# Kernel optimization log

Measured on AMD Instinct MI355X. Metric: run time of the kernel, lower is better.

Reference implementation:

```python
import jax, jax.numpy as jnp
import numpy as np

SEQ = 8192
D_IN = 1024
D_OUT = 128


def setup_inputs() -> dict:
    key = jax.random.key(0)
    k0, k1, k2, k3 = jax.random.split(key, 4)
    # kaiming-normal-ish init for weights (std = sqrt(2/fan_in))
    std = np.sqrt(2.0 / D_IN).astype(np.float32)
    return {
        "x": jax.random.normal(k0, (SEQ, D_IN), dtype=jnp.float32),
        "wq": jax.random.normal(k1, (D_IN, D_OUT), dtype=jnp.float32) * std,
        "wk": jax.random.normal(k2, (D_IN, D_OUT), dtype=jnp.float32) * std,
        "wv": jax.random.normal(k3, (D_IN, D_OUT), dtype=jnp.float32) * std,
    }


def reference(x, wq, wk, wv):
    # q,k,v: [S, d_out]
    q = x @ wq
    k = x @ wk
    v = x @ wv
    scale = jnp.sqrt(jnp.asarray(D_OUT, dtype=q.dtype))
    scores = (q @ k.T) / scale          # [S, S]
    attn = jax.nn.softmax(scores, axis=-1)
    return attn @ v                      # [S, d_out]
```

## Files before the change

### kernel.cpp

```cpp
#include <hip/hip_runtime.h>
#include <cstdint>

#define SEQ    8192
#define DIN    1024
#define DOUT   128
#define NSPLIT 8
#define KVTILE 64
#define QTILE  128
#define QK_SCALE 0.1275174246f
#define RESCALE_THR 8.0f

typedef unsigned short u16;
typedef __bf16 bf16x8 __attribute__((ext_vector_type(8)));
typedef float  f32x4  __attribute__((ext_vector_type(4)));
typedef float  f32x16 __attribute__((ext_vector_type(16)));
typedef unsigned short u16x8 __attribute__((ext_vector_type(8)));
typedef unsigned short u16x4 __attribute__((ext_vector_type(4)));
typedef unsigned int u32x2 __attribute__((ext_vector_type(2)));
typedef unsigned int u32x4 __attribute__((ext_vector_type(4)));

__device__ __forceinline__ u16 bfc(float f) {
  return __builtin_bit_cast(u16, (__bf16)f);
}
__device__ __forceinline__ float bf2f(u16 u) {
  union { uint32_t u; float f; } c; c.u = ((uint32_t)u) << 16; return c.f;
}

__device__ __forceinline__ bf16x8 ldsu8(const u16* base, int byteoff) {
  return __builtin_bit_cast(bf16x8,
    *reinterpret_cast<const u16x8*>(reinterpret_cast<const char*>(base) + byteoff));
}
__device__ __forceinline__ bf16x8 glbu8(const u16* p) {
  return __builtin_bit_cast(bf16x8, *reinterpret_cast<const u16x8*>(p));
}

__device__ __forceinline__ void gload_lds16(const void* g, void* l) {
  __builtin_amdgcn_global_load_lds(
      (const __attribute__((address_space(1))) void*)g,
      (__attribute__((address_space(3))) void*)l, 16, 0, 0);
}

__global__ __launch_bounds__(256) void k_wtrans(const float* __restrict__ wq,
                                                const float* __restrict__ wk,
                                                const float* __restrict__ wv,
                                                u16* __restrict__ Wt) {
  const float* w = (blockIdx.y == 0) ? wq : (blockIdx.y == 1) ? wk : wv;
  int idx = blockIdx.x * 256 + threadIdx.x;
  int k = idx >> 7, n = idx & 127;
  Wt[(size_t)blockIdx.y * (DOUT * DIN) + (size_t)n * DIN + k] = bfc(w[idx]);
}

__global__ __launch_bounds__(256) void k_xcast(const float* __restrict__ x,
                                               u16* __restrict__ Xb) {
  size_t base = ((size_t)blockIdx.x * 256 + threadIdx.x) * 8;
  float4 lo = *reinterpret_cast<const float4*>(x + base);
  float4 hi = *reinterpret_cast<const float4*>(x + base + 4);
  u16x8 v = { bfc(lo.x), bfc(lo.y), bfc(lo.z), bfc(lo.w),
              bfc(hi.x), bfc(hi.y), bfc(hi.z), bfc(hi.w) };
  *reinterpret_cast<u16x8*>(Xb + base) = v;
}

__global__ __launch_bounds__(256, 2) void k_gemm(const u16* __restrict__ Xb,
                                                 const u16* __restrict__ Wt,
                                                 u16* __restrict__ Q,
                                                 u16* __restrict__ K,
                                                 u16* __restrict__ Vt) {
  __shared__ __attribute__((aligned(16))) u16 As[2][64 * 128];
  __shared__ __attribute__((aligned(16))) u16 Bs[2][96 * 128];
  const int tid  = threadIdx.x;
  const int lane = tid & 63, wave = tid >> 6;
  const int lm   = lane & 15, g = lane >> 4;
  const int wm   = wave >> 1, wn = wave & 1;
  const int m0   = blockIdx.x * 64;
  const int n0   = blockIdx.y * 96;
  const int swzr = (lm & 7) << 4;

  const int trow = tid >> 4;
  const int tswz = ((tid & 15) << 4) ^ ((trow & 7) << 4);
  const char* baseA = (const char*)Xb + (size_t)(m0 + trow) * 2048 + tswz;
  const char* baseB = (const char*)Wt + (size_t)(n0 + trow) * 2048 + tswz;

  auto stage = [&](int buf, int kc) {
    const int kb = kc * 256;
#pragma unroll
    for (int i = 0; i < 4; ++i)
      gload_lds16(baseA + kb + i * 32768, &As[buf][i * 2048 + wave * 512]);
#pragma unroll
    for (int j = 0; j < 6; ++j)
      gload_lds16(baseB + kb + j * 32768, &Bs[buf][j * 2048 + wave * 512]);
  };

  f32x4 acc[2][3];
#pragma unroll
  for (int s = 0; s < 2; ++s)
#pragma unroll
    for (int nb = 0; nb < 3; ++nb) acc[s][nb] = (f32x4){0.f, 0.f, 0.f, 0.f};

  auto compute = [&](int buf) {
    const u16* As_ = As[buf];
    const u16* Bs_ = Bs[buf];
    bf16x8 a[2][4], b[3][4];
#pragma unroll
    for (int s = 0; s < 2; ++s)
#pragma unroll
      for (int t = 0; t < 4; ++t)
        a[s][t] = ldsu8(As_, (wm * 32 + s * 16 + lm) * 256 +
                             ((t * 64 + 16 * g) ^ swzr));
#pragma unroll
    for (int nb = 0; nb < 3; ++nb)
#pragma unroll
      for (int t = 0; t < 4; ++t)
        b[nb][t] = ldsu8(Bs_, (wn * 48 + nb * 16 + lm) * 256 +
                              ((t * 64 + 16 * g) ^ swzr));
#pragma unroll
    for (int s = 0; s < 2; ++s)
#pragma unroll
      for (int nb = 0; nb < 3; ++nb)
#pragma unroll
        for (int t = 0; t < 4; ++t)
          acc[s][nb] = __builtin_amdgcn_mfma_f32_16x16x32_bf16(
              a[s][t], b[nb][t], acc[s][nb], 0, 0, 0);
  };

  stage(0, 0);
  asm volatile("s_waitcnt vmcnt(0)" ::: "memory");
  __syncthreads();

#pragma unroll
  for (int kc = 0; kc < 8; kc += 2) {
    if (kc + 1 < 8) stage(1, kc + 1);
    compute(0);
    asm volatile("s_waitcnt vmcnt(0)" ::: "memory");
    __syncthreads();
    if (kc + 2 < 8) stage(0, kc + 2);
    compute(1);
    asm volatile("s_waitcnt vmcnt(0)" ::: "memory");
    __syncthreads();
  }

#pragma unroll
  for (int s = 0; s < 2; ++s)
#pragma unroll
    for (int nb = 0; nb < 3; ++nb) {
      int n = n0 + wn * 48 + nb * 16 + lm;
      int which = n >> 7, col = n & 127;
#pragma unroll
      for (int r = 0; r < 4; ++r) {
        int m = m0 + wm * 32 + s * 16 + g * 4 + r;
        if (which == 0)       Q[(size_t)m * DOUT + col] = bfc(acc[s][nb][r] * QK_SCALE);
        else if (which == 1)  K[(size_t)m * DOUT + col] = bfc(acc[s][nb][r]);
        else                  Vt[(size_t)col * SEQ + m] = bfc(acc[s][nb][r]);
      }
    }
}

__global__ __launch_bounds__(256, 2) void k_attn(const u16* __restrict__ Q,
                                                 const u16* __restrict__ K,
                                                 const u16* __restrict__ Vt,
                                                 u16* __restrict__ Op,
                                                 float* __restrict__ Mb,
                                                 float* __restrict__ Lb) {
  __shared__ __attribute__((aligned(16))) u16 Ks[2][64 * 128];
  __shared__ __attribute__((aligned(16))) u16 Vts[2][128 * 64];
  const int tid  = threadIdx.x;
  const int lane = tid & 63, wave = tid >> 6;
  const int l31  = lane & 31, h = lane >> 5;
  const int bid  = blockIdx.x;
  const int split = bid & 7;
  const int m0   = (bid >> 3) * QTILE;
  const int kvbase = split * (SEQ / NSPLIT);
  const int NIT = (SEQ / NSPLIT) / KVTILE;

  auto stage = [&](int buf, int kv0) {
#pragma unroll
    for (int i = 0; i < 4; ++i) {
      int krow = wave * 16 + i * 4 + (lane >> 4);
      const char* gk = (const char*)K + ((size_t)(kv0 + krow) << 8) +
                       (((lane & 15) << 4) ^ ((krow & 7) << 4));
      gload_lds16(gk, &Ks[buf][wave * 2048 + i * 512]);
      int vrow = wave * 32 + i * 8 + (lane >> 3);
      const char* gv = (const char*)Vt + (size_t)vrow * (SEQ * 2) +
                       (size_t)kv0 * 2 +
                       (((lane & 7) << 4) ^ ((vrow & 7) << 4));
      gload_lds16(gv, &Vts[buf][wave * 2048 + i * 512]);
    }
  };

  bf16x8 qf[8];
  stage(0, kvbase);
  {
    const u16* qp = Q + (size_t)(m0 + wave * 32 + l31) * DOUT + 8 * h;
#pragma unroll
    for (int t = 0; t < 8; ++t) qf[t] = glbu8(qp + t * 16);
  }
  asm volatile("s_waitcnt vmcnt(0)" ::: "memory");
  __syncthreads();

  f32x16 o[4] = {};
  float mr = -1e30f, lr = 0.f;

  int cur = 0;

  for (int it = 0; it < NIT; ++it) {
    if (it + 1 < NIT) stage(cur ^ 1, kvbase + (it + 1) * KVTILE);

    const u16* ks = Ks[cur];
    const u16* vs = Vts[cur];

    f32x16 s[2];
    __builtin_amdgcn_s_setprio(1);
#pragma unroll
    for (int kb = 0; kb < 2; ++kb) {
      f32x16 a = {};
      int krow = kb * 32 + l31;
      int rswz = (krow & 7) << 4;
#pragma unroll
      for (int t = 0; t < 8; ++t) {
        bf16x8 kf = ldsu8(ks, krow * 256 + ((t * 32 + 16 * h) ^ rswz));
        a = __builtin_amdgcn_mfma_f32_32x32x16_bf16(kf, qf[t], a, 0, 0, 0);
      }
      s[kb] = a;
    }
    __builtin_amdgcn_s_setprio(0);

    float t8[8];
#pragma unroll
    for (int i = 0; i < 8; ++i)
      t8[i] = fmaxf(fmaxf(s[0][2 * i], s[0][2 * i + 1]),
                    fmaxf(s[1][2 * i], s[1][2 * i + 1]));
    float u0 = fmaxf(fmaxf(t8[0], t8[1]), fmaxf(t8[2], t8[3]));
    float u1 = fmaxf(fmaxf(t8[4], t8[5]), fmaxf(t8[6], t8[7]));
    float rm = fmaxf(u0, u1);
    rm = fmaxf(rm, __shfl_xor(rm, 32));

    if (__any(rm - mr > RESCALE_THR)) {
      float mn = fmaxf(mr, rm);
      float alpha = exp2f(mr - mn);
      mr = mn;
      lr *= alpha;
#pragma unroll
      for (int db = 0; db < 4; ++db) o[db] *= alpha;
    }

    float rsum = 0.f;
#pragma unroll
    for (int j = 0; j < 4; ++j) {
      const int kb = j >> 1;
      const int base = (j & 1) * 8;
      float e0 = exp2f(s[kb][base + 0] - mr);
      float e1 = exp2f(s[kb][base + 1] - mr);
      float e2 = exp2f(s[kb][base + 2] - mr);
      float e3 = exp2f(s[kb][base + 3] - mr);
      float e4 = exp2f(s[kb][base + 4] - mr);
      float e5 = exp2f(s[kb][base + 5] - mr);
      float e6 = exp2f(s[kb][base + 6] - mr);
      float e7 = exp2f(s[kb][base + 7] - mr);
      rsum += ((e0 + e1) + (e2 + e3)) + ((e4 + e5) + (e6 + e7));
      u16x4 wa = { bfc(e0), bfc(e1), bfc(e2), bfc(e3) };
      u16x4 wb = { bfc(e4), bfc(e5), bfc(e6), bfc(e7) };
      u32x2 A = __builtin_bit_cast(u32x2, wa);
      u32x2 B = __builtin_bit_cast(u32x2, wb);
      u32x2 r01 = __builtin_amdgcn_permlane32_swap(A.x, B.x, false, false);
      u32x2 r23 = __builtin_amdgcn_permlane32_swap(A.y, B.y, false, false);
      u32x4 fr = { r01.x, r23.x, r01.y, r23.y };
      bf16x8 pb = __builtin_bit_cast(bf16x8, fr);
      __builtin_amdgcn_s_setprio(1);
#pragma unroll
      for (int db = 0; db < 4; ++db) {
        int vrow = db * 32 + l31;
        bf16x8 vb = ldsu8(vs, vrow * 128 +
                              ((32 * j + 16 * h) ^ ((vrow & 7) << 4)));
        o[db] = __builtin_amdgcn_mfma_f32_32x32x16_bf16(vb, pb, o[db], 0, 0, 0);
      }
      __builtin_amdgcn_s_setprio(0);
    }
    lr += rsum;

    asm volatile("s_waitcnt vmcnt(0)" ::: "memory");
    __syncthreads();
    cur ^= 1;
  }

  lr += __shfl_xor(lr, 32);

  const size_t ob = (size_t)split * SEQ * DOUT;
  const int q = m0 + wave * 32 + l31;
#pragma unroll
  for (int db = 0; db < 4; ++db)
#pragma unroll
    for (int j = 0; j < 4; ++j) {
      u16x4 w = { bfc(o[db][4 * j + 0]), bfc(o[db][4 * j + 1]),
                  bfc(o[db][4 * j + 2]), bfc(o[db][4 * j + 3]) };
      *reinterpret_cast<u16x4*>(Op + ob + (size_t)q * DOUT +
                                db * 32 + 8 * j + 4 * h) = w;
    }
  if (h == 0) {
    Mb[split * SEQ + q] = mr;
    Lb[split * SEQ + q] = lr;
  }
}

__global__ __launch_bounds__(256) void k_combine(const u16* __restrict__ Op,
                                                 const float* __restrict__ Mb,
                                                 const float* __restrict__ Lb,
                                                 float* __restrict__ out) {
  int idx = blockIdx.x * 256 + threadIdx.x;
  int srow = idx >> 7;
  float M = -1e30f;
#pragma unroll
  for (int s = 0; s < NSPLIT; ++s) M = fmaxf(M, Mb[s * SEQ + srow]);
  float num = 0.f, den = 0.f;
  const size_t st = (size_t)SEQ * DOUT;
#pragma unroll
  for (int s = 0; s < NSPLIT; ++s) {
    float e = exp2f(Mb[s * SEQ + srow] - M);
    den += Lb[s * SEQ + srow] * e;
    num += bf2f(Op[s * st + idx]) * e;
  }
  out[idx] = num / den;
}

extern "C" void kernel_launch(void* const* d_in, const int* in_sizes, int n_in,
                              void* d_out, int out_size, void* d_ws, size_t ws_size,
                              hipStream_t stream) {
  const float* x  = (const float*)d_in[0];
  const float* wq = (const float*)d_in[1];
  const float* wk = (const float*)d_in[2];
  const float* wv = (const float*)d_in[3];
  char* ws = (char*)d_ws;

  const size_t MB = (size_t)1 << 20;
  u16*   Wt = (u16*)(ws);
  u16*   Q  = (u16*)(ws + 768 * 1024);
  u16*   K  = (u16*)(ws + 768 * 1024 + 2 * MB);
  u16*   Vt = (u16*)(ws + 768 * 1024 + 4 * MB);
  float* Mb = (float*)(ws + 768 * 1024 + 6 * MB);
  float* Lb = (float*)(ws + 768 * 1024 + 6 * MB + 256 * 1024);
  u16*   Xb = (u16*)(ws + 7 * MB + 256 * 1024);
  u16*   Op = (u16*)(ws + 7 * MB + 256 * 1024);
  float* out = (float*)d_out;

  k_wtrans<<<dim3((DIN * DOUT) / 256, 3), 256, 0, stream>>>(wq, wk, wv, Wt);
  k_xcast<<<dim3((SEQ * DIN) / (256 * 8)), 256, 0, stream>>>(x, Xb);
  k_gemm<<<dim3(SEQ / 64, 4), 256, 0, stream>>>(Xb, Wt, Q, K, Vt);
  k_attn<<<dim3((SEQ / QTILE) * NSPLIT), 256, 0, stream>>>(Q, K, Vt, Op, Mb, Lb);
  k_combine<<<dim3((SEQ * DOUT) / 256), 256, 0, stream>>>(Op, Mb, Lb, out);
}
```

Baseline: 89.88 us.

## Software-pipeline QK and softmax-PV across KV tiles with smaller 2-wave blocks

```diff
diff --git a/kernel.cpp b/kernel.cpp
--- a/kernel.cpp
+++ b/kernel.cpp
@@ -5,8 +5,8 @@
 #define DIN    1024
 #define DOUT   128
 #define NSPLIT 8
-#define KVTILE 64
-#define QTILE  128
+#define KVTILE 32
+#define QTILE  64
 #define QK_SCALE 0.1275174246f
 #define RESCALE_THR 8.0f
 
@@ -154,14 +154,14 @@
     }
 }
 
-__global__ __launch_bounds__(256, 2) void k_attn(const u16* __restrict__ Q,
+__global__ __launch_bounds__(128, 2) void k_attn(const u16* __restrict__ Q,
                                                  const u16* __restrict__ K,
                                                  const u16* __restrict__ Vt,
                                                  u16* __restrict__ Op,
                                                  float* __restrict__ Mb,
                                                  float* __restrict__ Lb) {
-  __shared__ __attribute__((aligned(16))) u16 Ks[2][64 * 128];
-  __shared__ __attribute__((aligned(16))) u16 Vts[2][128 * 64];
+  __shared__ __attribute__((aligned(16))) u16 Ks[2][32 * 128];
+  __shared__ __attribute__((aligned(16))) u16 Vts[3][128 * 32];
   const int tid  = threadIdx.x;
   const int lane = tid & 63, wave = tid >> 6;
   const int l31  = lane & 31, h = lane >> 5;
@@ -171,68 +171,52 @@
   const int kvbase = split * (SEQ / NSPLIT);
   const int NIT = (SEQ / NSPLIT) / KVTILE;
 
-  auto stage = [&](int buf, int kv0) {
+  auto stageK = [&](int kb, int kv0) {
 #pragma unroll
     for (int i = 0; i < 4; ++i) {
       int krow = wave * 16 + i * 4 + (lane >> 4);
       const char* gk = (const char*)K + ((size_t)(kv0 + krow) << 8) +
                        (((lane & 15) << 4) ^ ((krow & 7) << 4));
-      gload_lds16(gk, &Ks[buf][wave * 2048 + i * 512]);
-      int vrow = wave * 32 + i * 8 + (lane >> 3);
+      gload_lds16(gk, &Ks[kb][wave * 2048 + i * 512]);
+    }
+  };
+  auto stageV = [&](u16* vbuf, int kv0) {
+#pragma unroll
+    for (int i = 0; i < 4; ++i) {
+      int vrow = wave * 64 + i * 16 + (lane >> 2);
       const char* gv = (const char*)Vt + (size_t)vrow * (SEQ * 2) +
                        (size_t)kv0 * 2 +
-                       (((lane & 7) << 4) ^ ((vrow & 7) << 4));
-      gload_lds16(gv, &Vts[buf][wave * 2048 + i * 512]);
+                       (((lane & 3) << 4) ^ (((vrow >> 1) & 3) << 4));
+      gload_lds16(gv, vbuf + wave * 2048 + i * 512);
     }
   };
 
   bf16x8 qf[8];
-  stage(0, kvbase);
-  {
-    const u16* qp = Q + (size_t)(m0 + wave * 32 + l31) * DOUT + 8 * h;
-#pragma unroll
-    for (int t = 0; t < 8; ++t) qf[t] = glbu8(qp + t * 16);
-  }
-  asm volatile("s_waitcnt vmcnt(0)" ::: "memory");
-  __syncthreads();
 
   f32x16 o[4] = {};
   float mr = -1e30f, lr = 0.f;
 
-  int cur = 0;
-
-  for (int it = 0; it < NIT; ++it) {
-    if (it + 1 < NIT) stage(cur ^ 1, kvbase + (it + 1) * KVTILE);
-
-    const u16* ks = Ks[cur];
-    const u16* vs = Vts[cur];
-
-    f32x16 s[2];
+  auto qk = [&](const u16* ks) -> f32x16 {
+    f32x16 a = {};
+    const int rswz = (l31 & 7) << 4;
     __builtin_amdgcn_s_setprio(1);
 #pragma unroll
-    for (int kb = 0; kb < 2; ++kb) {
-      f32x16 a = {};
-      int krow = kb * 32 + l31;
-      int rswz = (krow & 7) << 4;
-#pragma unroll
-      for (int t = 0; t < 8; ++t) {
-        bf16x8 kf = ldsu8(ks, krow * 256 + ((t * 32 + 16 * h) ^ rswz));
-        a = __builtin_amdgcn_mfma_f32_32x32x16_bf16(kf, qf[t], a, 0, 0, 0);
-      }
-      s[kb] = a;
+    for (int t = 0; t < 8; ++t) {
+      bf16x8 kf = ldsu8(ks, l31 * 256 + ((t * 32 + 16 * h) ^ rswz));
+      a = __builtin_amdgcn_mfma_f32_32x32x16_bf16(kf, qf[t], a, 0, 0, 0);
     }
     __builtin_amdgcn_s_setprio(0);
-
+    return a;
+  };
+
+  auto smpv = [&](f32x16 s, const u16* vs) {
     float t8[8];
 #pragma unroll
-    for (int i = 0; i < 8; ++i)
-      t8[i] = fmaxf(fmaxf(s[0][2 * i], s[0][2 * i + 1]),
-                    fmaxf(s[1][2 * i], s[1][2 * i + 1]));
+    for (int i = 0; i < 8; ++i) t8[i] = fmaxf(s[2 * i], s[2 * i + 1]);
     float u0 = fmaxf(fmaxf(t8[0], t8[1]), fmaxf(t8[2], t8[3]));
     float u1 = fmaxf(fmaxf(t8[4], t8[5]), fmaxf(t8[6], t8[7]));
     float rm = fmaxf(u0, u1);
     rm = fmaxf(rm, __shfl_xor(rm, 32));
-
     if (__any(rm - mr > RESCALE_THR)) {
       float mn = fmaxf(mr, rm);
       float alpha = exp2f(mr - mn);
@@ -241,20 +225,18 @@
 #pragma unroll
       for (int db = 0; db < 4; ++db) o[db] *= alpha;
     }
-
     float rsum = 0.f;
 #pragma unroll
-    for (int j = 0; j < 4; ++j) {
-      const int kb = j >> 1;
-      const int base = (j & 1) * 8;
-      float e0 = exp2f(s[kb][base + 0] - mr);
-      float e1 = exp2f(s[kb][base + 1] - mr);
-      float e2 = exp2f(s[kb][base + 2] - mr);
-      float e3 = exp2f(s[kb][base + 3] - mr);
-      float e4 = exp2f(s[kb][base + 4] - mr);
-      float e5 = exp2f(s[kb][base + 5] - mr);
-      float e6 = exp2f(s[kb][base + 6] - mr);
-      float e7 = exp2f(s[kb][base + 7] - mr);
+    for (int j = 0; j < 2; ++j) {
+      const int base = j * 8;
+      float e0 = exp2f(s[base + 0] - mr);
+      float e1 = exp2f(s[base + 1] - mr);
+      float e2 = exp2f(s[base + 2] - mr);
+      float e3 = exp2f(s[base + 3] - mr);
+      float e4 = exp2f(s[base + 4] - mr);
+      float e5 = exp2f(s[base + 5] - mr);
+      float e6 = exp2f(s[base + 6] - mr);
+      float e7 = exp2f(s[base + 7] - mr);
       rsum += ((e0 + e1) + (e2 + e3)) + ((e4 + e5) + (e6 + e7));
       u16x4 wa = { bfc(e0), bfc(e1), bfc(e2), bfc(e3) };
       u16x4 wb = { bfc(e4), bfc(e5), bfc(e6), bfc(e7) };
@@ -268,17 +250,50 @@
 #pragma unroll
       for (int db = 0; db < 4; ++db) {
         int vrow = db * 32 + l31;
-        bf16x8 vb = ldsu8(vs, vrow * 128 +
-                              ((32 * j + 16 * h) ^ ((vrow & 7) << 4)));
+        bf16x8 vb = ldsu8(vs, vrow * 64 +
+                              ((32 * j + 16 * h) ^ (((vrow >> 1) & 3) << 4)));
         o[db] = __builtin_amdgcn_mfma_f32_32x32x16_bf16(vb, pb, o[db], 0, 0, 0);
       }
       __builtin_amdgcn_s_setprio(0);
     }
     lr += rsum;
-
+  };
+
+  u16 *vA = Vts[0], *vB = Vts[1], *vC = Vts[2];
+  stageK(0, kvbase);
+  stageV(vA, kvbase);
+  stageK(1, kvbase + KVTILE);
+  stageV(vB, kvbase + KVTILE);
+  {
+    const u16* qp = Q + (size_t)(m0 + wave * 32 + l31) * DOUT + 8 * h;
+#pragma unroll
+    for (int t = 0; t < 8; ++t) qf[t] = glbu8(qp + t * 16);
+  }
+  asm volatile("s_waitcnt vmcnt(0)" ::: "memory");
+  __syncthreads();
+  f32x16 sA = qk(Ks[0]);
+  f32x16 sB;
+
+  for (int t = 0; t < NIT; t += 2) {
     asm volatile("s_waitcnt vmcnt(0)" ::: "memory");
     __syncthreads();
-    cur ^= 1;
+    if (t + 2 < NIT) {
+      stageK(0, kvbase + (t + 2) * KVTILE);
+      stageV(vC, kvbase + (t + 2) * KVTILE);
+    }
+    sB = qk(Ks[1]);
+    smpv(sA, vA);
+    { u16* tp = vA; vA = vB; vB = vC; vC = tp; }
+
+    asm volatile("s_waitcnt vmcnt(0)" ::: "memory");
+    __syncthreads();
+    if (t + 3 < NIT) {
+      stageK(1, kvbase + (t + 3) * KVTILE);
+      stageV(vC, kvbase + (t + 3) * KVTILE);
+    }
+    if (t + 2 < NIT) sA = qk(Ks[0]);
+    smpv(sB, vA);
+    { u16* tp = vA; vA = vB; vB = vC; vC = tp; }
   }
 
   lr += __shfl_xor(lr, 32);
@@ -343,6 +358,6 @@
   k_wtrans<<<dim3((DIN * DOUT) / 256, 3), 256, 0, stream>>>(wq, wk, wv, Wt);
   k_xcast<<<dim3((SEQ * DIN) / (256 * 8)), 256, 0, stream>>>(x, Xb);
   k_gemm<<<dim3(SEQ / 64, 4), 256, 0, stream>>>(Xb, Wt, Q, K, Vt);
-  k_attn<<<dim3((SEQ / QTILE) * NSPLIT), 256, 0, stream>>>(Q, K, Vt, Op, Mb, Lb);
+  k_attn<<<dim3((SEQ / QTILE) * NSPLIT), 128, 0, stream>>>(Q, K, Vt, Op, Mb, Lb);
   k_combine<<<dim3((SEQ * DOUT) / 256), 256, 0, stream>>>(Op, Mb, Lb, out);
 }
```

New measurement: 93.20 us. +3.7%, slower.
